# Kernel tuning notes

Measured on AMD Instinct MI355X. Metric: run time of the kernel, lower is better.

The kernel has to match this reference:

```python
import jax, jax.numpy as jnp
import numpy as np
from jax import lax

NUM_ENT = 100000
NUM_REL = 100          # init_rel has 2*NUM_REL rows (forward + inverse relations)
DIM = 200              # init_dim = gcn_dim = embed_dim
E = 1000000
B = 1024
K_H, K_W = 10, 20      # embed_dim == k_h * k_w
NUM_FILT = 200
KER = 7
FLAT_H = 2 * K_H - KER + 1   # 14
FLAT_W = K_W - KER + 1       # 14
FLAT_SZ = FLAT_H * FLAT_W * NUM_FILT  # 39200


def _bn1d(x, g, b, eps=1e-5):
    # training-mode BatchNorm1d (biased variance, matching torch)
    m = x.mean(0)
    v = x.var(0)
    return (x - m) * lax.rsqrt(v + eps) * g + b


def _bn2d(x, g, b, eps=1e-5):
    m = x.mean((0, 2, 3), keepdims=True)
    v = x.var((0, 2, 3), keepdims=True)
    return (x - m) * lax.rsqrt(v + eps) * g[None, :, None, None] + b[None, :, None, None]


def _compgcn_layer(x, r, src, dst, etype, enorm,
                   w_in, w_out, w_loop, w_rel, loop_rel, bias, gamma, beta):
    # CompGCNCov with opn='mult': comp(h_src, rel) = h_src * rel
    half = etype.shape[0] // 2
    comp = x[src] * r[etype]                                   # [E, din] edge gather + compose
    msg = jnp.concatenate([comp[:half] @ w_in,                 # first half: original edges
                           comp[half:] @ w_out], axis=0)       # second half: inverse edges
    msg = msg * enorm[:, None]
    agg = jax.ops.segment_sum(msg, dst, num_segments=NUM_ENT)  # scatter-sum to dst nodes
    loop = (x * loop_rel) @ w_loop                             # self-loop composition
    h = (agg + loop) * (1.0 / 3.0) + bias
    h = _bn1d(h, gamma, beta)
    return jnp.tanh(h), r @ w_rel


def setup_inputs() -> dict:
    key = jax.random.key(0)
    ks = jax.random.split(key, 40)
    f32 = jnp.float32
    s = 1.0 / np.sqrt(DIM)
    inp = {
        "init_embed": jax.random.normal(ks[0], (NUM_ENT, DIM), f32) * s,
        "init_rel":   jax.random.normal(ks[1], (2 * NUM_REL, DIM), f32) * s,
        "edge_norm":  jax.random.uniform(ks[2], (E,), f32),
    }
    names = ["w_in", "w_out", "w_loop", "w_rel"]
    for layer in (1, 2):
        for i, n in enumerate(names):
            inp[f"{n}{layer}"] = jax.random.normal(ks[3 + 6 * layer + i], (DIM, DIM), f32) * s
        inp[f"loop_rel{layer}"] = jax.random.normal(jax.random.fold_in(key, layer), (1, DIM), f32) * s
        inp[f"b{layer}"] = jnp.zeros((DIM,), f32)
        inp[f"g{layer}"] = jnp.ones((DIM,), f32)
        inp[f"be{layer}"] = jnp.zeros((DIM,), f32)
    inp["conv_w"] = jax.random.normal(ks[20], (NUM_FILT, 1, KER, KER), f32) * (1.0 / KER)
    inp["conv_b"] = jnp.zeros((NUM_FILT,), f32)
    inp["fc_w"] = jax.random.normal(ks[21], (DIM, FLAT_SZ), f32) * (1.0 / np.sqrt(FLAT_SZ))
    inp["fc_b"] = jnp.zeros((DIM,), f32)
    for n, c in (("bn0", 1), ("bn1", NUM_FILT), ("bn2", DIM)):
        inp[f"{n}_g"] = jnp.ones((c,), f32)
        inp[f"{n}_b"] = jnp.zeros((c,), f32)
    inp["subj"] = jax.random.randint(ks[22], (B,), 0, NUM_ENT)
    inp["rel_idx"] = jax.random.randint(ks[23], (B,), 0, 2 * NUM_REL)
    inp["obj"] = jax.random.randint(ks[24], (B,), 0, NUM_ENT)
    inp["src"] = jax.random.randint(ks[25], (E,), 0, NUM_ENT)
    inp["dst"] = jax.random.randint(ks[26], (E,), 0, NUM_ENT)
    inp["edge_type"] = jnp.concatenate([
        jax.random.randint(ks[27], (E // 2,), 0, NUM_REL),          # in-edges
        jax.random.randint(ks[28], (E // 2,), NUM_REL, 2 * NUM_REL)])  # inverse edges
    return inp


def reference(init_embed, init_rel, edge_norm,
              w_in1, w_out1, w_loop1, w_rel1, loop_rel1, b1, g1, be1,
              w_in2, w_out2, w_loop2, w_rel2, loop_rel2, b2, g2, be2,
              conv_w, conv_b, fc_w, fc_b,
              bn0_g, bn0_b, bn1_g, bn1_b, bn2_g, bn2_b,
              subj, rel_idx, obj, src, dst, edge_type):
    # --- GCN encoder: 2 CompGCN layers ---
    x, r = _compgcn_layer(init_embed, init_rel, src, dst, edge_type, edge_norm,
                          w_in1, w_out1, w_loop1, w_rel1, loop_rel1, b1, g1, be1)
    x, r = _compgcn_layer(x, r, src, dst, edge_type, edge_norm,
                          w_in2, w_out2, w_loop2, w_rel2, loop_rel2, b2, g2, be2)
    sub_emb, rel_emb, obj_emb = x[subj], r[rel_idx], x[obj]   # [B, DIM] each
    # --- ConvE scoring head ---
    stk = jnp.concatenate([sub_emb[:, None, :], rel_emb[:, None, :]], 1)
    stk = stk.reshape(B, 1, 2 * K_H, K_W)                     # [B,1,20,20]
    h = _bn2d(stk, bn0_g, bn0_b)
    h = lax.conv_general_dilated(h, conv_w, (1, 1), 'VALID',
                                 dimension_numbers=('NCHW', 'OIHW', 'NCHW'))
    h = h + conv_b[None, :, None, None]                       # [B,NUM_FILT,14,14]
    h = jnp.maximum(_bn2d(h, bn1_g, bn1_b), 0.0)
    h = h.reshape(B, FLAT_SZ) @ fc_w.T + fc_b                 # [B, DIM]
    h = jnp.maximum(_bn1d(h, bn2_g, bn2_b), 0.0)
    return jax.nn.sigmoid(h @ obj_emb.T)                      # [B, B]
```

## Files before the change

### kernel.cpp

```cpp
#include <hip/hip_runtime.h>

#define DIM 200
#define NENT 100000
#define NEDGE 1000000
#define EHALF 500000
#define NB 1024
#define NFILT 200
#define FLATSZ 39200

#define NDF ((size_t)NENT * DIM)
#define REGF ((size_t)20100000)

#define PANEL_TOT_H 6656
#define Y1OFF_H 3584
#define WT_TOTAL_H 139776

typedef float floatx4 __attribute__((ext_vector_type(4)));
typedef _Float16 halfx8 __attribute__((ext_vector_type(8)));
typedef _Float16 halfx4 __attribute__((ext_vector_type(4)));

__device__ __forceinline__ void gAtomicAdd(float* p, float v) { unsafeAtomicAdd(p, v); }
__device__ __forceinline__ void gAtomicAdd(double* p, double v) { unsafeAtomicAdd(p, v); }

__device__ __forceinline__ void gload16h(const _Float16* g, _Float16* l) {
    __builtin_amdgcn_global_load_lds(
        (const __attribute__((address_space(1))) void*)g,
        (__attribute__((address_space(3))) void*)l,
        16, 0, 0);
}

__global__ __launch_bounds__(256) void edge_hist(
    const int* __restrict__ dst, int* __restrict__ hist)
{
    int stride = gridDim.x * blockDim.x;
    for (int e = blockIdx.x * 256 + threadIdx.x; e < NEDGE; e += stride)
        atomicAdd(&hist[dst[e]], 1);
}

__global__ __launch_bounds__(256) void scan1(
    const int* __restrict__ hist, int* __restrict__ incl, int* __restrict__ bsum)
{
    __shared__ int sm[256];
    int i = blockIdx.x * 256 + threadIdx.x;
    int t = threadIdx.x;
    sm[t] = (i < NENT) ? hist[i] : 0;
    __syncthreads();
    for (int off = 1; off < 256; off <<= 1) {
        int v = (t >= off) ? sm[t - off] : 0;
        __syncthreads();
        sm[t] += v;
        __syncthreads();
    }
    if (i < NENT) incl[i] = sm[t];
    if (t == 255) bsum[blockIdx.x] = sm[255];
}

__global__ __launch_bounds__(512) void scan2(int* bsum, int nb)
{
    __shared__ int sm[512];
    int t = threadIdx.x;
    int v = (t < nb) ? bsum[t] : 0;
    sm[t] = v;
    __syncthreads();
    for (int off = 1; off < 512; off <<= 1) {
        int u = (t >= off) ? sm[t - off] : 0;
        __syncthreads();
        sm[t] += u;
        __syncthreads();
    }
    if (t < nb) bsum[t] = sm[t] - v;
}

__global__ __launch_bounds__(256) void scan3(
    const int* __restrict__ hist, int* __restrict__ offs,
    const int* __restrict__ bsum, int* __restrict__ cursor)
{
    int i = blockIdx.x * 256 + threadIdx.x;
    if (i < NENT) {
        int excl = offs[i] - hist[i] + bsum[blockIdx.x];
        offs[i] = excl;
        cursor[i] = excl;
    }
    if (i == 0) offs[NENT] = NEDGE;
}

__global__ __launch_bounds__(256) void edge_fill(
    const int* __restrict__ src, const int* __restrict__ dst,
    const int* __restrict__ etype, const float* __restrict__ enorm,
    int* __restrict__ cursor, uint2* __restrict__ recs)
{
    int stride = gridDim.x * blockDim.x;
    for (int e = blockIdx.x * 256 + threadIdx.x; e < NEDGE; e += stride) {
        int pos = atomicAdd(&cursor[dst[e]], 1);
        union { _Float16 h; unsigned short s; } wc;
        wc.h = (_Float16)enorm[e];
        unsigned a = (unsigned)(src[e] * 400) | ((e >= EHALF) ? 0x80000000u : 0u);
        unsigned b = (unsigned)etype[e] | ((unsigned)wc.s << 16);
        recs[pos] = make_uint2(a, b);
    }
}

__global__ __launch_bounds__(256) void build_map(
    const int* __restrict__ subj, const int* __restrict__ obj, int* __restrict__ map)
{
    int i = blockIdx.x * 256 + threadIdx.x;
    if (i < NB) map[subj[i]] = i;
    else if (i < 2 * NB) map[obj[i - NB]] = i;
}

__global__ __launch_bounds__(256) void to_f16(
    const float* __restrict__ X, _Float16* __restrict__ Y, long n4)
{
    long stride = (long)gridDim.x * blockDim.x;
    for (long i = (long)blockIdx.x * blockDim.x + threadIdx.x; i < n4; i += stride) {
        float4 v = ((const float4*)X)[i];
        halfx4 h;
        h[0] = (_Float16)v.x; h[1] = (_Float16)v.y;
        h[2] = (_Float16)v.z; h[3] = (_Float16)v.w;
        ((halfx4*)Y)[i] = h;
    }
}

__global__ __launch_bounds__(256) void to_f16_pad(
    const float* __restrict__ X, _Float16* __restrict__ Y)
{
    int i = blockIdx.x * 256 + threadIdx.x;
    if (i >= 40000) return;
    int row = i / 200, col = i - row * 200;
    Y[row * 256 + col] = (_Float16)X[i];
}

__global__ __launch_bounds__(256) void gather_nodes(
    const _Float16* __restrict__ x16, const _Float16* __restrict__ r16p,
    const int* __restrict__ offs, const uint2* __restrict__ recs,
    _Float16* __restrict__ aggI, _Float16* __restrict__ aggO)
{
    int node = __builtin_amdgcn_readfirstlane(blockIdx.x * 4 + (threadIdx.x >> 6));
    int lane = threadIdx.x & 63;
    if (node >= NENT) return;
    int beg = offs[node], end = offs[node + 1];
    bool act = lane < 50;
    int lane_c = min(lane, 49);
    unsigned lo = (unsigned)(lane_c * 8);
    const char* xb = (const char*)x16;
    const char* rb = (const char*)r16p;
    halfx4 aI = (halfx4)0, aO = (halfx4)0;

    if (beg < end) {
        uint2 rcA = recs[beg];
        uint2 rcB = recs[min(beg + 1, end - 1)];
        halfx4 xvA = *(const halfx4*)(xb + ((rcA.x & 0x7FFFFFFFu) + lo));
        halfx4 rvA = *(const halfx4*)(rb + (((rcA.y & 0x1FFu) << 9) + lo));
        for (int i = beg; i < end; ++i) {
            uint2 rcC = recs[min(i + 2, end - 1)];
            halfx4 xvB = *(const halfx4*)(xb + ((rcB.x & 0x7FFFFFFFu) + lo));
            halfx4 rvB = *(const halfx4*)(rb + (((rcB.y & 0x1FFu) << 9) + lo));
            union { unsigned u; _Float16 h[2]; } wu; wu.u = rcA.y;
            _Float16 wh = wu.h[1];
            halfx4 w4 = {wh, wh, wh, wh};
            halfx4 comp = xvA * rvA;
            if ((int)rcA.x < 0) aO += comp * w4;
            else aI += comp * w4;
            rcA = rcB; rcB = rcC; xvA = xvB; rvA = rvB;
        }
    }
    if (act) {
        size_t base = (size_t)node * 200 + lane * 4;
        *(halfx4*)&aggI[base] = aI;
        *(halfx4*)&aggO[base] = aO;
    }
}

__global__ __launch_bounds__(256) void pack_w3(
    const float* __restrict__ w0, const float* __restrict__ w1,
    const float* __restrict__ w2, const float* __restrict__ lrel,
    _Float16* __restrict__ WpP)
{
    int i = blockIdx.x * 256 + threadIdx.x;
    if (i >= WT_TOTAL_H) return;
    int p = i / PANEL_TOT_H;
    int r = i % PANEL_TOT_H;
    int y = (r >= Y1OFF_H) ? 1 : 0;
    int rr = y ? (r - Y1OFF_H) : r;
    int rl = rr >> 5;
    int qx = (rr >> 3) & 3;
    int e = rr & 7;
    int q = qx ^ ((rl >> 1) & 3);
    int n = y * 112 + rl;
    int seg = p / 7, c = p - seg * 7;
    int k = c * 32 + q * 8 + e;
    const float* W = (seg == 0) ? w0 : (seg == 1) ? w1 : w2;
    float v = (n < 200 && k < 200) ? W[k * 200 + n] : 0.f;
    if (seg == 2 && n < 200 && k < 200) v *= lrel[k];
    WpP[i] = (_Float16)v;
}

__global__ __launch_bounds__(256) void pack_fcw(
    const float* __restrict__ W, _Float16* __restrict__ Wt)
{
    long i = (long)blockIdx.x * 256 + threadIdx.x;
    if (i >= (long)208 * FLATSZ) return;
    int n = (int)(i / FLATSZ);
    Wt[i] = (n < 200) ? (_Float16)W[i] : (_Float16)0.f;
}

template<int Y>
__global__ __launch_bounds__(1024) void gemm_big(
    const _Float16* __restrict__ A0h, const _Float16* __restrict__ A1h,
    const _Float16* __restrict__ A2h, const _Float16* __restrict__ WpP,
    float* __restrict__ C, const float* __restrict__ bias,
    const int* __restrict__ map, float alpha,
    double* __restrict__ s1, double* __restrict__ s2)
{
    constexpr int NF = Y ? 6 : 7;
    constexpr int PC = NF;
    constexpr int PANEL_H = NF * 512;
    constexpr int YOFF_H = Y ? Y1OFF_H : 0;
    constexpr int SEG_LDS_H = 7 * PANEL_H;
    __shared__ _Float16 Sb[2 * SEG_LDS_H];
    __shared__ float fsum[NF * 16];
    __shared__ float fsq[NF * 16];

    int tid = threadIdx.x;
    int lane = tid & 63, wave = tid >> 6;
    int col16 = lane & 15, quad = lane >> 4;
    if (tid < NF * 16) { fsum[tid] = 0.f; fsq[tid] = 0.f; }

    int gw = blockIdx.x * 16 + wave;
    bool act = gw < 3125;
    int t = act ? gw : 0;
    int r0 = t * 32 + col16, r1 = r0 + 16;
    size_t b0 = (size_t)r0 * 200, b1 = (size_t)r1 * 200;

    floatx4 acc[NF][2];
#pragma unroll
    for (int nf = 0; nf < NF; ++nf) { acc[nf][0] = (floatx4)0.f; acc[nf][1] = (floatx4)0.f; }

    halfx8 ca0, ca1, na0, na1;

    auto stage = [&](int seg, int bufi) {
        for (int cc = wave; cc < 7 * PC; cc += 16) {
            int p7 = cc / PC, sub = cc - p7 * PC;
            const _Float16* g = WpP + (size_t)(seg * 7 + p7) * PANEL_TOT_H
                              + YOFF_H + sub * 512 + lane * 8;
            gload16h(g, Sb + bufi * SEG_LDS_H + cc * 512);
        }
    };
    auto loadA = [&](int kc, halfx8& a0, halfx8& a1) {
        int seg = kc / 7, c = kc - seg * 7;
        int koff = c * 32 + quad * 8;
        if (koff < 200) {
            const _Float16* A = (seg == 0) ? A0h : (seg == 1) ? A1h : A2h;
            a0 = *(const halfx8*)&A[b0 + koff];
            a1 = *(const halfx8*)&A[b1 + koff];
        } else {
            a0 = (halfx8)0; a1 = (halfx8)0;
        }
    };

    stage(0, 0);
    if (act) loadA(0, ca0, ca1);
    __syncthreads();

    int buf = 0;
    for (int seg = 0; seg < 3; ++seg) {
        if (seg < 2) stage(seg + 1, buf ^ 1);
        if (act) {
#pragma unroll
            for (int c = 0; c < 7; ++c) {
                int kc = seg * 7 + c;
                if (kc < 20) loadA(kc + 1, na0, na1);
                const _Float16* P = Sb + buf * SEG_LDS_H + c * PANEL_H;
                __builtin_amdgcn_s_setprio(1);
#pragma unroll
                for (int nf = 0; nf < NF; ++nf) {
                    int rl = nf * 16 + col16;
                    int qs = quad ^ ((rl >> 1) & 3);
                    halfx8 b = *(const halfx8*)&P[rl * 32 + qs * 8];
                    acc[nf][0] = __builtin_amdgcn_mfma_f32_16x16x32_f16(ca0, b, acc[nf][0], 0, 0, 0);
                    acc[nf][1] = __builtin_amdgcn_mfma_f32_16x16x32_f16(ca1, b, acc[nf][1], 0, 0, 0);
                }
                __builtin_amdgcn_s_setprio(0);
                ca0 = na0; ca1 = na1;
            }
        }
        __syncthreads();
        buf ^= 1;
    }

    int slot[2][4];
    if (map && act) {
#pragma unroll
        for (int h = 0; h < 2; ++h)
#pragma unroll
            for (int j = 0; j < 4; ++j)
                slot[h][j] = map[t * 32 + h * 16 + quad * 4 + j];
    }
    if (act) {
#pragma unroll
        for (int nf = 0; nf < NF; ++nf) {
            int lc = nf * 16 + col16;
            int colg = Y * 112 + lc;
            float ls = 0.f, lq = 0.f;
            if (colg < 200) {
                float bv = bias[colg];
#pragma unroll
                for (int h = 0; h < 2; ++h) {
                    int rbase = t * 32 + h * 16 + quad * 4;
#pragma unroll
                    for (int j = 0; j < 4; ++j) {
                        float v = acc[nf][h][j] * alpha + bv;
                        ls += v; lq += v * v;
                        if (!map) {
                            C[(size_t)(rbase + j) * 200 + colg] = v;
                        } else {
                            int s = slot[h][j];
                            if (s >= 0) C[(size_t)s * 200 + colg] = v;
                        }
                    }
                }
            }
            ls += __shfl_down(ls, 32); ls += __shfl_down(ls, 16);
            lq += __shfl_down(lq, 32); lq += __shfl_down(lq, 16);
            if (quad == 0 && colg < 200) {
                atomicAdd(&fsum[lc], ls);
                atomicAdd(&fsq[lc], lq);
            }
        }
    }
    __syncthreads();
    if (tid < NF * 16) {
        int colg = Y * 112 + tid;
        if (colg < 200) {
            gAtomicAdd(&s1[colg], (double)fsum[tid]);
            gAtomicAdd(&s2[colg], (double)fsq[tid]);
        }
    }
}

template<int NF0, int NF>
__device__ __forceinline__ void fc_gemm_body(
    const _Float16* __restrict__ Ph, const _Float16* __restrict__ Wt,
    float* __restrict__ part, int ky, _Float16* Bs)
{
    int t = threadIdx.x;
    int lane = t & 63, wave = t >> 6;
    int col16 = lane & 15, quad = lane >> 4;
    int row_base = blockIdx.x * 128 + wave * 32;
    int c0 = ky * 25;
    floatx4 acc[NF][2];
#pragma unroll
    for (int nf = 0; nf < NF; ++nf) { acc[nf][0] = (floatx4)0.f; acc[nf][1] = (floatx4)0.f; }
    int r0 = row_base + col16, r1 = row_base + 16 + col16;
    const int rows4 = NF * 16 * 4;

    for (int c = c0; c < c0 + 25; ++c) {
        int k0 = c * 32;
        for (int i = t; i < rows4; i += 256) {
            int nl = i >> 2, part_i = i & 3;
            int n = NF0 * 16 + nl;
            *(halfx8*)&Bs[nl * 40 + part_i * 8] =
                *(const halfx8*)&Wt[(size_t)n * FLATSZ + k0 + part_i * 8];
        }
        __syncthreads();
        int koff = k0 + quad * 8;
        halfx8 a0 = *(const halfx8*)&Ph[(size_t)r0 * FLATSZ + koff];
        halfx8 a1 = *(const halfx8*)&Ph[(size_t)r1 * FLATSZ + koff];
#pragma unroll
        for (int nf = 0; nf < NF; ++nf) {
            halfx8 b = *(const halfx8*)&Bs[(nf * 16 + col16) * 40 + quad * 8];
            acc[nf][0] = __builtin_amdgcn_mfma_f32_16x16x32_f16(a0, b, acc[nf][0], 0, 0, 0);
            acc[nf][1] = __builtin_amdgcn_mfma_f32_16x16x32_f16(a1, b, acc[nf][1], 0, 0, 0);
        }
        __syncthreads();
    }
    float* out = part + (size_t)ky * (NB * 200);
#pragma unroll
    for (int nf = 0; nf < NF; ++nf) {
        int colg = NF0 * 16 + nf * 16 + col16;
        if (colg >= 200) continue;
#pragma unroll
        for (int h = 0; h < 2; ++h) {
            int rbase = row_base + h * 16 + quad * 4;
#pragma unroll
            for (int j = 0; j < 4; ++j)
                out[(size_t)(rbase + j) * 200 + colg] = acc[nf][h][j];
        }
    }
}

__global__ __launch_bounds__(256) void fc_gemm(
    const _Float16* __restrict__ Ph, const _Float16* __restrict__ Wt,
    float* __restrict__ part)
{
    __shared__ _Float16 Bs[112 * 40];
    int ky = blockIdx.y >> 1;
    if ((blockIdx.y & 1) == 0)
        fc_gemm_body<0, 7>(Ph, Wt, part, ky, Bs);
    else
        fc_gemm_body<7, 6>(Ph, Wt, part, ky, Bs);
}

__global__ __launch_bounds__(256) void fc_reduce(
    const float* __restrict__ part, const float* __restrict__ bias,
    float* __restrict__ hfc)
{
    int i = blockIdx.x * 256 + threadIdx.x;
    float acc = bias[i % 200];
#pragma unroll
    for (int y = 0; y < 49; ++y) acc += part[(size_t)y * (NB * 200) + i];
    hfc[i] = acc;
}

__global__ __launch_bounds__(256) void colstats(
    const float* __restrict__ X, int M, int rpb,
    double* __restrict__ s1, double* __restrict__ s2)
{
    int c = threadIdx.x;
    if (c >= 200) return;
    int r0 = blockIdx.x * rpb;
    int r1 = min(r0 + rpb, M);
    float sum = 0.f, sq = 0.f;
    for (int rr = r0; rr < r1; ++rr) {
        float v = X[(size_t)rr * 200 + c];
        sum += v; sq += v * v;
    }
    gAtomicAdd(&s1[c], (double)sum);
    gAtomicAdd(&s2[c], (double)sq);
}

__global__ void finalize_stats(const double* __restrict__ s1, const double* __restrict__ s2,
                               const float* __restrict__ g, const float* __restrict__ bb,
                               float* __restrict__ sc, float* __restrict__ sh,
                               int ncols, double count)
{
    int c = threadIdx.x;
    if (c >= ncols) return;
    double m = s1[c] / count;
    double v = s2[c] / count - m * m;
    double scd = (double)g[c] / sqrt(v + 1e-5);
    sc[c] = (float)scd;
    sh[c] = (float)((double)bb[c] - m * scd);
}

__global__ __launch_bounds__(256) void bn_tanh_f16(
    const float* __restrict__ X, const float* __restrict__ sc,
    const float* __restrict__ sh, _Float16* __restrict__ Y, long n4)
{
    long stride = (long)gridDim.x * blockDim.x;
    for (long i = (long)blockIdx.x * blockDim.x + threadIdx.x; i < n4; i += stride) {
        int c4 = (int)(i % 50) * 4;
        float4 v = ((const float4*)X)[i];
        halfx4 h;
        h[0] = (_Float16)tanhf(v.x * sc[c4 + 0] + sh[c4 + 0]);
        h[1] = (_Float16)tanhf(v.y * sc[c4 + 1] + sh[c4 + 1]);
        h[2] = (_Float16)tanhf(v.z * sc[c4 + 2] + sh[c4 + 2]);
        h[3] = (_Float16)tanhf(v.w * sc[c4 + 3] + sh[c4 + 3]);
        ((halfx4*)Y)[i] = h;
    }
}

__global__ __launch_bounds__(256) void bn_act_200(
    float* __restrict__ X, const float* __restrict__ sc, const float* __restrict__ sh,
    long n4, int act)
{
    long stride = (long)gridDim.x * blockDim.x;
    for (long i = (long)blockIdx.x * blockDim.x + threadIdx.x; i < n4; i += stride) {
        int c4 = (int)(i % 50) * 4;
        float4 v = ((const float4*)X)[i];
        float a0 = v.x * sc[c4 + 0] + sh[c4 + 0];
        float a1 = v.y * sc[c4 + 1] + sh[c4 + 1];
        float a2 = v.z * sc[c4 + 2] + sh[c4 + 2];
        float a3 = v.w * sc[c4 + 3] + sh[c4 + 3];
        if (act == 0) { a0 = tanhf(a0); a1 = tanhf(a1); a2 = tanhf(a2); a3 = tanhf(a3); }
        else { a0 = fmaxf(a0, 0.f); a1 = fmaxf(a1, 0.f); a2 = fmaxf(a2, 0.f); a3 = fmaxf(a3, 0.f); }
        ((float4*)X)[i] = make_float4(a0, a1, a2, a3);
    }
}

__global__ __launch_bounds__(256) void rel_mm(
    const float* __restrict__ R, const float* __restrict__ W, float* __restrict__ O)
{
    int idx = blockIdx.x * blockDim.x + threadIdx.x;
    if (idx >= 200 * 200) return;
    int row = idx / 200, col = idx - row * 200;
    float acc = 0.f;
    for (int k = 0; k < 200; ++k) acc = fmaf(R[row * 200 + k], W[k * 200 + col], acc);
    O[idx] = acc;
}

__global__ __launch_bounds__(256) void build_stk(
    const float* __restrict__ x2c, const float* __restrict__ r2,
    const int* __restrict__ subj, const int* __restrict__ ridx,
    const int* __restrict__ map,
    float* __restrict__ stk, double* __restrict__ s1, double* __restrict__ s2)
{
    __shared__ float wsum[4], wsq[4];
    int b = blockIdx.x, t = threadIdx.x;
    const float* se = x2c + (size_t)map[subj[b]] * DIM;
    const float* re = r2 + (size_t)ridx[b] * DIM;
    float sum = 0.f, sq = 0.f;
    for (int i = t; i < 400; i += 256) {
        float v = (i < 200) ? se[i] : re[i - 200];
        stk[(size_t)b * 400 + i] = v;
        sum += v; sq += v * v;
    }
    for (int off = 32; off > 0; off >>= 1) {
        sum += __shfl_down(sum, off);
        sq  += __shfl_down(sq, off);
    }
    if ((t & 63) == 0) { wsum[t >> 6] = sum; wsq[t >> 6] = sq; }
    __syncthreads();
    if (t == 0) {
        float S = wsum[0] + wsum[1] + wsum[2] + wsum[3];
        float Q = wsq[0] + wsq[1] + wsq[2] + wsq[3];
        gAtomicAdd(&s1[0], (double)S);
        gAtomicAdd(&s2[0], (double)Q);
    }
}

__global__ __launch_bounds__(256) void conv_fwd(
    const float* __restrict__ stk, const float* __restrict__ conv_w,
    const float* __restrict__ conv_b, const float* __restrict__ sc0,
    const float* __restrict__ sh0, _Float16* __restrict__ Ph,
    double* __restrict__ s1, double* __restrict__ s2)
{
    __shared__ float img[400];
    __shared__ float wsm[9800];
    __shared__ float bsm[200];
    __shared__ float fsum[200];
    __shared__ float fsq[200];
    int b = blockIdx.x, t = threadIdx.x;
    float scale0 = sc0[0], shift0 = sh0[0];
    if (t < 200) { fsum[t] = 0.f; fsq[t] = 0.f; bsm[t] = conv_b[t]; }
    for (int i = t; i < 400; i += 256) img[i] = stk[(size_t)b * 400 + i] * scale0 + shift0;
    for (int i = t; i < 9800; i += 256) wsm[i] = conv_w[i];
    __syncthreads();
    for (int fy = t; fy < 2800; fy += 256) {
        int f = fy / 14, y = fy - (fy / 14) * 14;
        const float* wf = &wsm[f * 49];
        float acc[14];
        float bias = bsm[f];
#pragma unroll
        for (int xx = 0; xx < 14; ++xx) acc[xx] = bias;
#pragma unroll
        for (int i = 0; i < 7; ++i) {
            const float* rowp = &img[(y + i) * 20];
            float rv[20];
#pragma unroll
            for (int c = 0; c < 20; ++c) rv[c] = rowp[c];
#pragma unroll
            for (int j = 0; j < 7; ++j) {
                float wv = wf[i * 7 + j];
#pragma unroll
                for (int xx = 0; xx < 14; ++xx) acc[xx] = fmaf(rv[xx + j], wv, acc[xx]);
            }
        }
        float ls = 0.f, lq = 0.f;
        _Float16* pp = Ph + (size_t)b * FLATSZ + (size_t)f * 196 + y * 14;
#pragma unroll
        for (int xx = 0; xx < 14; ++xx) {
            float v = acc[xx];
            pp[xx] = (_Float16)v;
            ls += v; lq += v * v;
        }
        atomicAdd(&fsum[f], ls);
        atomicAdd(&fsq[f], lq);
    }
    __syncthreads();
    if (t < 200) {
        gAtomicAdd(&s1[t], (double)fsum[t]);
        gAtomicAdd(&s2[t], (double)fsq[t]);
    }
}

__global__ __launch_bounds__(256) void bn1_relu_f16(
    _Float16* __restrict__ Ph, const float* __restrict__ sc, const float* __restrict__ sh)
{
    long n4 = (long)NB * (FLATSZ / 4);
    long stride = (long)gridDim.x * blockDim.x;
    for (long i = (long)blockIdx.x * blockDim.x + threadIdx.x; i < n4; i += stride) {
        int k4 = (int)(i % (FLATSZ / 4));
        int f = k4 / 49;
        float s = sc[f], h = sh[f];
        halfx4 v = ((const halfx4*)Ph)[i];
#pragma unroll
        for (int e = 0; e < 4; ++e) {
            float x = (float)v[e];
            x = fmaxf(x * s + h, 0.f);
            v[e] = (_Float16)x;
        }
        ((halfx4*)Ph)[i] = v;
    }
}

__global__ __launch_bounds__(256) void score_mm(
    const float* __restrict__ Hn, const float* __restrict__ x2c,
    const int* __restrict__ obj, const int* __restrict__ map,
    float* __restrict__ out)
{
    __shared__ float Asm[16][17];
    __shared__ float Bsm[16][17];
    int tx = threadIdx.x & 15, ty = threadIdx.x >> 4;
    int row = blockIdx.y * 16 + ty;
    int col = blockIdx.x * 16 + tx;
    int oj = map[obj[blockIdx.x * 16 + ty]];
    float acc = 0.f;
    for (int k0 = 0; k0 < 200; k0 += 16) {
        int k = k0 + tx;
        Asm[ty][tx] = (k < 200) ? Hn[(size_t)row * 200 + k] : 0.f;
        Bsm[ty][tx] = (k < 200) ? x2c[(size_t)oj * 200 + k] : 0.f;
        __syncthreads();
#pragma unroll
        for (int kk = 0; kk < 16; ++kk) acc = fmaf(Asm[ty][kk], Bsm[tx][kk], acc);
        __syncthreads();
    }
    out[(size_t)row * NB + col] = 1.f / (1.f + expf(-acc));
}

extern "C" void kernel_launch(void* const* d_in, const int* in_sizes, int n_in,
                              void* d_out, int out_size, void* d_ws, size_t ws_size,
                              hipStream_t stream)
{
    (void)in_sizes; (void)n_in; (void)out_size;
    const float* init_embed = (const float*)d_in[0];
    const float* init_rel   = (const float*)d_in[1];
    const float* edge_norm  = (const float*)d_in[2];
    const float* w_in1  = (const float*)d_in[3];
    const float* w_out1 = (const float*)d_in[4];
    const float* w_loop1= (const float*)d_in[5];
    const float* w_rel1 = (const float*)d_in[6];
    const float* lrel1  = (const float*)d_in[7];
    const float* b1     = (const float*)d_in[8];
    const float* gm1    = (const float*)d_in[9];
    const float* be1    = (const float*)d_in[10];
    const float* w_in2  = (const float*)d_in[11];
    const float* w_out2 = (const float*)d_in[12];
    const float* w_loop2= (const float*)d_in[13];
    const float* w_rel2 = (const float*)d_in[14];
    const float* lrel2  = (const float*)d_in[15];
    const float* b2     = (const float*)d_in[16];
    const float* gm2    = (const float*)d_in[17];
    const float* be2    = (const float*)d_in[18];
    const float* conv_w = (const float*)d_in[19];
    const float* conv_b = (const float*)d_in[20];
    const float* fc_w   = (const float*)d_in[21];
    const float* fc_b   = (const float*)d_in[22];
    const float* bn0_g  = (const float*)d_in[23];
    const float* bn0_b  = (const float*)d_in[24];
    const float* bn1_g  = (const float*)d_in[25];
    const float* bn1_b  = (const float*)d_in[26];
    const float* bn2_g  = (const float*)d_in[27];
    const float* bn2_b  = (const float*)d_in[28];
    const int* subj   = (const int*)d_in[29];
    const int* relidx = (const int*)d_in[30];
    const int* obj    = (const int*)d_in[31];
    const int* src    = (const int*)d_in[32];
    const int* dst    = (const int*)d_in[33];
    const int* etype  = (const int*)d_in[34];

    float* ws = (float*)d_ws;
    float* R0 = ws;
    float* R1 = ws + REGF;
    float* R2 = ws + 2 * REGF;
    float* p = ws + 3 * REGF;
    float* r1v = p;            p += 40000;
    float* r2v = p;            p += 40000;
    float* stk = p;            p += 409600;
    float* hfc = p;            p += 204800;
    float* x2c = p;            p += 409600;
    float* fsc = p;            p += 256;
    float* fsh = p;            p += 256;
    double* ds1 = (double*)p;  p += 512;
    double* ds2 = (double*)p;  p += 512;
    _Float16* Wp = (_Float16*)p; p += (WT_TOTAL_H + 1) / 2;
    _Float16* rg16p = (_Float16*)p; p += 25600;
    int* map = (int*)p;        p += NENT;
    int* hist = (int*)p;       p += NENT;
    int* offs = (int*)p;       p += NENT + 4;
    int* cursor = (int*)p;     p += NENT;
    int* bsum = (int*)p;       p += 512;
    uint2* recs = (uint2*)p;   p += (size_t)NEDGE * 2;

    float* x1f = R0;
    _Float16* aggI1 = (_Float16*)R1;
    _Float16* ie16  = (_Float16*)(R1 + 10050000);
    _Float16* aggOh = (_Float16*)R2;
    _Float16* x1h = (_Float16*)R1;
    _Float16* aggI2 = (_Float16*)R0;
    _Float16* Ph  = (_Float16*)R0;
    _Float16* fch = (_Float16*)R2;
    float* fpart = R2 + 4200000;

    const size_t NEED = (size_t)(p - ws) * sizeof(float);
    if (ws_size < NEED) return;

    const int NBLK = (NENT + 255) / 256;
    const size_t DSBYTES = 512 * sizeof(double);

    hipMemsetAsync(hist, 0, NENT * sizeof(int), stream);
    hipMemsetAsync(map, 0xFF, NENT * sizeof(int), stream);
    edge_hist<<<1024, 256, 0, stream>>>(dst, hist);
    scan1<<<NBLK, 256, 0, stream>>>(hist, offs, bsum);
    scan2<<<1, 512, 0, stream>>>(bsum, NBLK);
    scan3<<<NBLK, 256, 0, stream>>>(hist, offs, bsum, cursor);
    edge_fill<<<1024, 256, 0, stream>>>(src, dst, etype, edge_norm, cursor, recs);
    build_map<<<(2 * NB + 255) / 256, 256, 0, stream>>>(subj, obj, map);

    const int PACK_BLKS = (WT_TOTAL_H + 255) / 256;

    pack_w3<<<PACK_BLKS, 256, 0, stream>>>(w_in1, w_out1, w_loop1, lrel1, Wp);
    to_f16<<<4096, 256, 0, stream>>>(init_embed, ie16, (long)NENT * 50);
    to_f16_pad<<<157, 256, 0, stream>>>(init_rel, rg16p);
    gather_nodes<<<(NENT + 3) / 4, 256, 0, stream>>>(ie16, rg16p, offs, recs,
                                                     aggI1, aggOh);
    hipMemsetAsync(ds1, 0, DSBYTES, stream);
    gemm_big<0><<<256, 1024, 0, stream>>>(aggI1, aggOh, ie16, Wp,
                                          x1f, b1, nullptr, 1.f / 3.f, ds1, ds2);
    gemm_big<1><<<256, 1024, 0, stream>>>(aggI1, aggOh, ie16, Wp,
                                          x1f, b1, nullptr, 1.f / 3.f, ds1, ds2);
    finalize_stats<<<1, 256, 0, stream>>>(ds1, ds2, gm1, be1, fsc, fsh, 200, (double)NENT);
    bn_tanh_f16<<<4096, 256, 0, stream>>>(x1f, fsc, fsh, x1h, (long)NENT * 50);
    rel_mm<<<(40000 + 255) / 256, 256, 0, stream>>>(init_rel, w_rel1, r1v);

    pack_w3<<<PACK_BLKS, 256, 0, stream>>>(w_in2, w_out2, w_loop2, lrel2, Wp);
    to_f16_pad<<<157, 256, 0, stream>>>(r1v, rg16p);
    gather_nodes<<<(NENT + 3) / 4, 256, 0, stream>>>(x1h, rg16p, offs, recs,
                                                     aggI2, aggOh);
    hipMemsetAsync(ds1, 0, DSBYTES, stream);
    gemm_big<0><<<256, 1024, 0, stream>>>(aggI2, aggOh, x1h, Wp,
                                          x2c, b2, map, 1.f / 3.f, ds1, ds2);
    gemm_big<1><<<256, 1024, 0, stream>>>(aggI2, aggOh, x1h, Wp,
                                          x2c, b2, map, 1.f / 3.f, ds1, ds2);
    finalize_stats<<<1, 256, 0, stream>>>(ds1, ds2, gm2, be2, fsc, fsh, 200, (double)NENT);
    bn_act_200<<<400, 256, 0, stream>>>(x2c, fsc, fsh, (long)2 * NB * 50, 0);
    rel_mm<<<(40000 + 255) / 256, 256, 0, stream>>>(r1v, w_rel2, r2v);

    hipMemsetAsync(ds1, 0, DSBYTES, stream);
    build_stk<<<NB, 256, 0, stream>>>(x2c, r2v, subj, relidx, map, stk, ds1, ds2);
    finalize_stats<<<1, 256, 0, stream>>>(ds1, ds2, bn0_g, bn0_b, fsc, fsh, 1,
                                          (double)((long)NB * 400));
    hipMemsetAsync(ds1, 0, DSBYTES, stream);
    conv_fwd<<<NB, 256, 0, stream>>>(stk, conv_w, conv_b, fsc, fsh, Ph, ds1, ds2);
    finalize_stats<<<1, 256, 0, stream>>>(ds1, ds2, bn1_g, bn1_b, fsc, fsh, 200,
                                          (double)((long)NB * 196));
    bn1_relu_f16<<<4096, 256, 0, stream>>>(Ph, fsc, fsh);
    pack_fcw<<<(int)(((long)208 * FLATSZ + 255) / 256), 256, 0, stream>>>(fc_w, fch);
    fc_gemm<<<dim3(8, 98), 256, 0, stream>>>(Ph, fch, fpart);
    fc_reduce<<<800, 256, 0, stream>>>(fpart, fc_b, hfc);
    hipMemsetAsync(ds1, 0, DSBYTES, stream);
    colstats<<<4, 256, 0, stream>>>(hfc, NB, 256, ds1, ds2);
    finalize_stats<<<1, 256, 0, stream>>>(ds1, ds2, bn2_g, bn2_b, fsc, fsh, 200, (double)NB);
    bn_act_200<<<200, 256, 0, stream>>>(hfc, fsc, fsh, (long)NB * 50, 1);
    score_mm<<<dim3(NB / 16, NB / 16), 256, 0, stream>>>(hfc, x2c, obj, map, (float*)d_out);
}
```

Before: 1.033 ms.

## Map one thread per conv filter with register-resident weights in conv_fwd

```diff
diff --git a/kernel.cpp b/kernel.cpp
--- a/kernel.cpp
+++ b/kernel.cpp
@@ -526,21 +526,22 @@
     double* __restrict__ s1, double* __restrict__ s2)
 {
     __shared__ float img[400];
-    __shared__ float wsm[9800];
-    __shared__ float bsm[200];
-    __shared__ float fsum[200];
-    __shared__ float fsq[200];
     int b = blockIdx.x, t = threadIdx.x;
     float scale0 = sc0[0], shift0 = sh0[0];
-    if (t < 200) { fsum[t] = 0.f; fsq[t] = 0.f; bsm[t] = conv_b[t]; }
-    for (int i = t; i < 400; i += 256) img[i] = stk[(size_t)b * 400 + i] * scale0 + shift0;
-    for (int i = t; i < 9800; i += 256) wsm[i] = conv_w[i];
+    for (int i = t; i < 400; i += 256)
+        img[i] = stk[(size_t)b * 400 + i] * scale0 + shift0;
     __syncthreads();
-    for (int fy = t; fy < 2800; fy += 256) {
-        int f = fy / 14, y = fy - (fy / 14) * 14;
-        const float* wf = &wsm[f * 49];
+    if (t >= 200) return;
+
+    float w[49];
+#pragma unroll
+    for (int i = 0; i < 49; ++i) w[i] = conv_w[t * 49 + i];
+    float bias = conv_b[t];
+    float ls = 0.f, lq = 0.f;
+    _Float16* pp = Ph + (size_t)b * FLATSZ + (size_t)t * 196;
+
+    for (int y = 0; y < 14; ++y) {
         float acc[14];
-        float bias = bsm[f];
 #pragma unroll
         for (int xx = 0; xx < 14; ++xx) acc[xx] = bias;
 #pragma unroll
@@ -548,30 +549,28 @@
             const float* rowp = &img[(y + i) * 20];
             float rv[20];
 #pragma unroll
-            for (int c = 0; c < 20; ++c) rv[c] = rowp[c];
+            for (int c4 = 0; c4 < 5; ++c4) {
+                float4 v4 = *(const float4*)&rowp[c4 * 4];
+                rv[c4 * 4 + 0] = v4.x; rv[c4 * 4 + 1] = v4.y;
+                rv[c4 * 4 + 2] = v4.z; rv[c4 * 4 + 3] = v4.w;
+            }
 #pragma unroll
             for (int j = 0; j < 7; ++j) {
-                float wv = wf[i * 7 + j];
-#pragma unroll
-                for (int xx = 0; xx < 14; ++xx) acc[xx] = fmaf(rv[xx + j], wv, acc[xx]);
+                float wv = w[i * 7 + j];
+#pragma unroll
+                for (int xx = 0; xx < 14; ++xx)
+                    acc[xx] = fmaf(rv[xx + j], wv, acc[xx]);
             }
         }
-        float ls = 0.f, lq = 0.f;
-        _Float16* pp = Ph + (size_t)b * FLATSZ + (size_t)f * 196 + y * 14;
 #pragma unroll
         for (int xx = 0; xx < 14; ++xx) {
             float v = acc[xx];
-            pp[xx] = (_Float16)v;
+            pp[y * 14 + xx] = (_Float16)v;
             ls += v; lq += v * v;
         }
-        atomicAdd(&fsum[f], ls);
-        atomicAdd(&fsq[f], lq);
-    }
-    __syncthreads();
-    if (t < 200) {
-        gAtomicAdd(&s1[t], (double)fsum[t]);
-        gAtomicAdd(&s2[t], (double)fsq[t]);
-    }
+    }
+    gAtomicAdd(&s1[t], (double)ls);
+    gAtomicAdd(&s2[t], (double)lq);
 }
 
 __global__ __launch_bounds__(256) void bn1_relu_f16(
```

Measured after the change: 1.068 ms. +3.5%, slower.
